# Kernel optimization log

Measured on AMD Instinct MI355X. Metric: run time of the kernel, lower is better.

The kernel has to match this reference:

```python
import jax, jax.numpy as jnp
import numpy as np

B, N, IN_DIM, OUT_DIM = 8, 2048, 128, 128
NEG_SLOPE = 0.2

def setup_inputs() -> dict:
    key = jax.random.key(0)
    k1, k2, k3, k4 = jax.random.split(key, 4)
    x = jax.random.normal(k1, (B, N, IN_DIM), dtype=jnp.float32)
    adj = jax.random.randint(k2, (N, N), 0, 2, dtype=jnp.int32)
    # nn.Linear weight init scale ~ 1/sqrt(fan_in)
    W = jax.random.normal(k3, (IN_DIM, OUT_DIM), dtype=jnp.float32) / np.sqrt(IN_DIM)
    a_vec = jax.random.normal(k4, (2 * OUT_DIM,), dtype=jnp.float32) / np.sqrt(2 * OUT_DIM)
    return {"x": x, "adj": adj, "W": W, "a_vec": a_vec}

def reference(x, adj, W, a_vec):
    # h = x @ W : [b, n, d]
    h = jnp.einsum("bni,io->bno", x, W)
    # Algebraic decomposition of a([h_i, h_j]) = a1.h_i + a2.h_j
    a1, a2 = a_vec[:OUT_DIM], a_vec[OUT_DIM:]
    s_i = h @ a1  # [b, n] score contribution from source node i
    s_j = h @ a2  # [b, n] score contribution from target node j
    e = s_i[:, :, None] + s_j[:, None, :]  # [b, n, n]
    e = jnp.where(e >= 0, e, NEG_SLOPE * e)  # leaky_relu(0.2)
    mask = (adj > 0)[None, :, :]  # [1, n, n] broadcast over batch
    e = jnp.where(mask, e, -jnp.inf)
    alpha = jax.nn.softmax(e, axis=-1)  # [b, n, n]
    out = jnp.einsum("bnm,bmd->bnd", alpha, h)  # [b, n, d]
    return out, alpha
```

## Files before the change

### kernel.cpp

```cpp
#include <hip/hip_runtime.h>
#include <hip/hip_bf16.h>
#include <cstdint>
#include <cstddef>

constexpr int Bn = 8;
constexpr int Nn = 2048;
constexpr int Dn = 128;

typedef __bf16 bf16x8 __attribute__((ext_vector_type(8)));
typedef float f32x4 __attribute__((ext_vector_type(4)));

#define AS1 __attribute__((address_space(1)))
#define AS3 __attribute__((address_space(3)))

static __device__ __forceinline__ void gl_lds16(const void* g, void* l) {
  __builtin_amdgcn_global_load_lds((AS1 const void*)g, (AS3 void*)l, 16, 0, 0);
}

__global__ __launch_bounds__(256) void gat_k0(
    const int* __restrict__ adj, unsigned long long* __restrict__ mask64) {
  const int t = threadIdx.x;
  const size_t g = (size_t)blockIdx.x * 256 + t;
  int v = adj[g];
  unsigned long long bal = __ballot(v > 0);
  if ((t & 63) == 0) mask64[g >> 6] = bal;
}

__global__ __launch_bounds__(256) void gat_k1(
    const float* __restrict__ x, const float* __restrict__ W,
    const float* __restrict__ a_vec,
    __bf16* __restrict__ hT, float* __restrict__ s1, float* __restrict__ s2) {
  __shared__ __align__(16) float Wl[64 * 144];
  __shared__ __align__(16) float xL[32 * 132];

  const int t = threadIdx.x;
  const int r0 = blockIdx.x * 32;
  const int b = r0 >> 11;
  const int n0 = r0 & (Nn - 1);
  const int rp = (t >> 4) << 1;
  const int c0 = (t & 15) << 3;
  const int c0p = c0 + ((c0 >> 5) << 2);

  float acc[2][8];
#pragma unroll
  for (int r = 0; r < 2; ++r)
#pragma unroll
    for (int c = 0; c < 8; ++c) acc[r][c] = 0.f;

#pragma unroll
  for (int it = 0; it < 4; ++it) {
    int idx = t + (it << 8);
    int rr = idx >> 5, kc = (idx & 31) << 2;
    *(float4*)(xL + rr * 132 + kc) = *(const float4*)(x + (size_t)(r0 + rr) * Dn + kc);
  }

  for (int ph = 0; ph < 2; ++ph) {
    if (ph) __syncthreads();
#pragma unroll
    for (int it = 0; it < 8; ++it) {
      int idx = t + (it << 8);
      int kk = idx >> 5, c4 = (idx & 31) << 2;
      int dsto = kk * 144 + c4 + ((c4 >> 5) << 2);
      *(float4*)(Wl + dsto) = *(const float4*)(W + (size_t)((ph << 6) + kk) * Dn + c4);
    }
    __syncthreads();
    const float* xrow = xL + rp * 132 + (ph << 6);
    for (int k = 0; k < 64; ++k) {
      float xa0 = xrow[k];
      float xa1 = xrow[132 + k];
      float4 w0 = *(const float4*)(Wl + k * 144 + c0p);
      float4 w1 = *(const float4*)(Wl + k * 144 + c0p + 4);
      float ws[8] = {w0.x, w0.y, w0.z, w0.w, w1.x, w1.y, w1.z, w1.w};
#pragma unroll
      for (int c = 0; c < 8; ++c) {
        acc[0][c] = fmaf(xa0, ws[c], acc[0][c]);
        acc[1][c] = fmaf(xa1, ws[c], acc[1][c]);
      }
    }
  }

  float q1[2] = {0.f, 0.f}, q2[2] = {0.f, 0.f};
#pragma unroll
  for (int c = 0; c < 8; ++c) {
    float a1c = a_vec[c0 + c];
    float a2c = a_vec[Dn + c0 + c];
    q1[0] = fmaf(acc[0][c], a1c, q1[0]);
    q1[1] = fmaf(acc[1][c], a1c, q1[1]);
    q2[0] = fmaf(acc[0][c], a2c, q2[0]);
    q2[1] = fmaf(acc[1][c], a2c, q2[1]);
  }
#pragma unroll
  for (int d = 1; d < 16; d <<= 1) {
    q1[0] += __shfl_xor(q1[0], d);
    q1[1] += __shfl_xor(q1[1], d);
    q2[0] += __shfl_xor(q2[0], d);
    q2[1] += __shfl_xor(q2[1], d);
  }
  if ((t & 15) == 0) {
    s1[b * Nn + n0 + rp] = q1[0];
    s1[b * Nn + n0 + rp + 1] = q1[1];
    s2[b * Nn + n0 + rp] = q2[0];
    s2[b * Nn + n0 + rp + 1] = q2[1];
  }

#pragma unroll
  for (int c = 0; c < 8; ++c) {
    union { __bf16 h[2]; uint32_t u; } pk;
    pk.h[0] = (__bf16)acc[0][c];
    pk.h[1] = (__bf16)acc[1][c];
    *(uint32_t*)(hT + (size_t)(b * Dn + c0 + c) * Nn + n0 + rp) = pk.u;
  }
}

__global__ __launch_bounds__(512) void gat_k2(
    const uint32_t* __restrict__ mask, const __bf16* __restrict__ hT,
    const float* __restrict__ s1, const float* __restrict__ s2,
    float* __restrict__ out, float* __restrict__ alpha) {
  __shared__ __align__(16) float sj[Nn];
  __shared__ float siv[32], invl[32];
  __shared__ __align__(16) __bf16 Pl[2][32 * 72];
  __shared__ __align__(16) __bf16 hl[2][128 * 64];

  const int t = threadIdx.x;
  const int b = blockIdx.x & 7;
  const int i0 = (blockIdx.x >> 3) << 5;
  const int w = t >> 6, lane = t & 63;
  const int ii = t >> 4, sub = t & 15;
  const int lrow = lane >> 3, ccs = lane & 7;
  const __bf16* __restrict__ hTb = hT + (size_t)b * Dn * Nn;

#pragma unroll
  for (int inst = 0; inst < 2; ++inst) {
    int row = (w << 4) + (inst << 3) + lrow;
    gl_lds16(hTb + (size_t)row * Nn + ((ccs ^ lrow) << 3),
             &hl[0][((w << 4) + (inst << 3)) << 6]);
  }

  *(float4*)(sj + (t << 2)) = *(const float4*)(s2 + b * Nn + (t << 2));
  if (t < 32) siv[t] = s1[b * Nn + i0 + t];
  __syncthreads();

  const int i = i0 + ii;
  const uint32_t* __restrict__ mrow = mask + ((size_t)i << 6);
  const float si = siv[ii];

  float l = 0.f;
  const int wofs = sub >> 3;
  const int bsh = (sub & 7) << 2;
  for (int cc = 0; cc < 32; ++cc) {
    int j = (cc << 6) + (sub << 2);
    uint32_t mw = mrow[(cc << 1) + wofs];
    float4 sv = *(const float4*)(sj + j);
    float e;
    e = si + sv.x; e = fmaxf(e, 0.2f * e); l += ((mw >> (bsh + 0)) & 1u) ? __expf(e) : 0.f;
    e = si + sv.y; e = fmaxf(e, 0.2f * e); l += ((mw >> (bsh + 1)) & 1u) ? __expf(e) : 0.f;
    e = si + sv.z; e = fmaxf(e, 0.2f * e); l += ((mw >> (bsh + 2)) & 1u) ? __expf(e) : 0.f;
    e = si + sv.w; e = fmaxf(e, 0.2f * e); l += ((mw >> (bsh + 3)) & 1u) ? __expf(e) : 0.f;
  }
  l += __shfl_xor(l, 1);
  l += __shfl_xor(l, 2);
  l += __shfl_xor(l, 4);
  l += __shfl_xor(l, 8);
  if (sub == 0) invl[ii] = 1.f / l;
  __syncthreads();
  const float il = invl[ii];

  const int iw = (w & 1) << 4;
  const int nd0 = (w >> 1) << 5;
  const int q16 = lane >> 4, m16 = lane & 15;
  f32x4 acc0 = {0.f, 0.f, 0.f, 0.f}, acc1 = {0.f, 0.f, 0.f, 0.f};
  float* __restrict__ arow = alpha + ((size_t)(b * Nn + i) << 11);

  for (int jt = 0; jt < 32; ++jt) {
    const int buf = jt & 1;
    const int j0 = jt << 6;
    {
      int j = j0 + (sub << 2);
      uint32_t mw = mrow[(j0 >> 5) + wofs];
      float4 sv = *(const float4*)(sj + j);
      float e0 = si + sv.x; e0 = fmaxf(e0, 0.2f * e0);
      float e1 = si + sv.y; e1 = fmaxf(e1, 0.2f * e1);
      float e2 = si + sv.z; e2 = fmaxf(e2, 0.2f * e2);
      float e3 = si + sv.w; e3 = fmaxf(e3, 0.2f * e3);
      float a0 = ((mw >> (bsh + 0)) & 1u) ? __expf(e0) * il : 0.f;
      float a1 = ((mw >> (bsh + 1)) & 1u) ? __expf(e1) * il : 0.f;
      float a2 = ((mw >> (bsh + 2)) & 1u) ? __expf(e2) * il : 0.f;
      float a3 = ((mw >> (bsh + 3)) & 1u) ? __expf(e3) * il : 0.f;
      *(float4*)(arow + j) = make_float4(a0, a1, a2, a3);
      union { __bf16 h[4]; uint2 u; } pk;
      pk.h[0] = (__bf16)a0; pk.h[1] = (__bf16)a1;
      pk.h[2] = (__bf16)a2; pk.h[3] = (__bf16)a3;
      *(uint2*)(&Pl[buf][ii * 72 + (sub << 2)]) = pk.u;
    }
    __syncthreads();
    if (jt < 31) {
      int jn = j0 + 64;
#pragma unroll
      for (int inst = 0; inst < 2; ++inst) {
        int row = (w << 4) + (inst << 3) + lrow;
        gl_lds16(hTb + (size_t)row * Nn + jn + ((ccs ^ lrow) << 3),
                 &hl[buf ^ 1][((w << 4) + (inst << 3)) << 6]);
      }
    }
#pragma unroll
    for (int ks = 0; ks < 2; ++ks) {
      bf16x8 af = *(const bf16x8*)(&Pl[buf][(iw + m16) * 72 + (ks << 5) + (q16 << 3)]);
      {
        int d = nd0 + m16;
        int phys = ((ks << 2) + q16) ^ (d & 7);
        bf16x8 bv = *(const bf16x8*)(&hl[buf][(d << 6) + (phys << 3)]);
        acc0 = __builtin_amdgcn_mfma_f32_16x16x32_bf16(af, bv, acc0, 0, 0, 0);
      }
      {
        int d = nd0 + 16 + m16;
        int phys = ((ks << 2) + q16) ^ (d & 7);
        bf16x8 bv = *(const bf16x8*)(&hl[buf][(d << 6) + (phys << 3)]);
        acc1 = __builtin_amdgcn_mfma_f32_16x16x32_bf16(af, bv, acc1, 0, 0, 0);
      }
    }
  }

#pragma unroll
  for (int nb = 0; nb < 2; ++nb) {
    f32x4 a = nb ? acc1 : acc0;
    int d = nd0 + (nb << 4) + m16;
#pragma unroll
    for (int r = 0; r < 4; ++r) {
      int irow = i0 + iw + (q16 << 2) + r;
      out[((size_t)(b * Nn + irow) << 7) + d] = a[r];
    }
  }
}

extern "C" void kernel_launch(void* const* d_in, const int* in_sizes, int n_in,
                              void* d_out, int out_size, void* d_ws, size_t ws_size,
                              hipStream_t stream) {
  const float* x = (const float*)d_in[0];
  const int* adj = (const int*)d_in[1];
  const float* W = (const float*)d_in[2];
  const float* a_vec = (const float*)d_in[3];

  float* out = (float*)d_out;
  float* alpha = out + (size_t)Bn * Nn * Dn;

  char* ws = (char*)d_ws;
  __bf16* hT = (__bf16*)ws;
  float* s1 = (float*)(ws + (size_t)Bn * Dn * Nn * 2);
  float* s2 = s1 + (size_t)Bn * Nn;
  unsigned long long* mask64 = (unsigned long long*)(s2 + (size_t)Bn * Nn);

  gat_k0<<<(Nn * Nn) / 256, 256, 0, stream>>>(adj, mask64);
  gat_k1<<<512, 256, 0, stream>>>(x, W, a_vec, hT, s1, s2);
  gat_k2<<<512, 512, 0, stream>>>((const uint32_t*)mask64, hT, s1, s2, out, alpha);
}
```

Before: 200.9 us.

## Split alpha writing into separate blocks and fuse mask packing into projection kernel

The adjacency mask packing moves into the projection kernel, so the standalone mask kernel disappears. The softmax row sums now come from a new small kernel that writes 1/l to the workspace. The main kernel no longer writes the 128 MB alpha matrix from its MFMA loop. Instead, 1024 extra blocks in the same launch recompute and write alpha with nontemporal stores, running in parallel with the P·h matmul blocks. The aim is to stop the large alpha store from stalling the matmul pipeline, at the cost of recomputing the exponentials and adding one more launch.

```diff
diff --git a/kernel.cpp b/kernel.cpp
--- a/kernel.cpp
+++ b/kernel.cpp
@@ -17,19 +17,11 @@
   __builtin_amdgcn_global_load_lds((AS1 const void*)g, (AS3 void*)l, 16, 0, 0);
 }
 
-__global__ __launch_bounds__(256) void gat_k0(
-    const int* __restrict__ adj, unsigned long long* __restrict__ mask64) {
-  const int t = threadIdx.x;
-  const size_t g = (size_t)blockIdx.x * 256 + t;
-  int v = adj[g];
-  unsigned long long bal = __ballot(v > 0);
-  if ((t & 63) == 0) mask64[g >> 6] = bal;
-}
-
 __global__ __launch_bounds__(256) void gat_k1(
     const float* __restrict__ x, const float* __restrict__ W,
-    const float* __restrict__ a_vec,
-    __bf16* __restrict__ hT, float* __restrict__ s1, float* __restrict__ s2) {
+    const float* __restrict__ a_vec, const int* __restrict__ adj,
+    __bf16* __restrict__ hT, float* __restrict__ s1, float* __restrict__ s2,
+    unsigned long long* __restrict__ mask64) {
   __shared__ __align__(16) float Wl[64 * 144];
   __shared__ __align__(16) float xL[32 * 132];
 
@@ -110,18 +102,96 @@
     pk.h[1] = (__bf16)acc[1][c];
     *(uint32_t*)(hT + (size_t)(b * Dn + c0 + c) * Nn + n0 + rp) = pk.u;
   }
-}
-
-__global__ __launch_bounds__(512) void gat_k2(
+
+  {
+    const size_t base = (size_t)blockIdx.x * 8192;
+#pragma unroll 4
+    for (int it = 0; it < 32; ++it) {
+      size_t g = base + (it << 8) + t;
+      int v = adj[g];
+      unsigned long long bal = __ballot(v > 0);
+      if ((t & 63) == 0) mask64[g >> 6] = bal;
+    }
+  }
+}
+
+__global__ __launch_bounds__(256) void gat_k2a(
+    const uint32_t* __restrict__ mask, const float* __restrict__ s1,
+    const float* __restrict__ s2, float* __restrict__ invl_g) {
+  __shared__ __align__(16) float sj[Nn];
+  const int t = threadIdx.x;
+  const int b = blockIdx.x & 7;
+  const int i0 = (blockIdx.x >> 3) << 5;
+#pragma unroll
+  for (int it = 0; it < 2; ++it) {
+    int idx = (t + (it << 8)) << 2;
+    *(float4*)(sj + idx) = *(const float4*)(s2 + b * Nn + idx);
+  }
+  __syncthreads();
+
+  const int ii = t >> 3, sub = t & 7;
+  const int i = i0 + ii;
+  const uint32_t* __restrict__ mrow = mask + ((size_t)i << 6);
+  const float si = s1[b * Nn + i];
+  const int bsh = sub << 2;
+
+  float l = 0.f;
+  for (int cc = 0; cc < 64; ++cc) {
+    uint32_t mw = mrow[cc];
+    float4 sv = *(const float4*)(sj + (cc << 5) + bsh);
+    float e;
+    e = si + sv.x; e = fmaxf(e, 0.2f * e); l += ((mw >> (bsh + 0)) & 1u) ? __expf(e) : 0.f;
+    e = si + sv.y; e = fmaxf(e, 0.2f * e); l += ((mw >> (bsh + 1)) & 1u) ? __expf(e) : 0.f;
+    e = si + sv.z; e = fmaxf(e, 0.2f * e); l += ((mw >> (bsh + 2)) & 1u) ? __expf(e) : 0.f;
+    e = si + sv.w; e = fmaxf(e, 0.2f * e); l += ((mw >> (bsh + 3)) & 1u) ? __expf(e) : 0.f;
+  }
+  l += __shfl_xor(l, 1);
+  l += __shfl_xor(l, 2);
+  l += __shfl_xor(l, 4);
+  if (sub == 0) invl_g[b * Nn + i] = 1.f / l;
+}
+
+__global__ __launch_bounds__(512) void gat_k2bc(
     const uint32_t* __restrict__ mask, const __bf16* __restrict__ hT,
     const float* __restrict__ s1, const float* __restrict__ s2,
+    const float* __restrict__ invl_g,
     float* __restrict__ out, float* __restrict__ alpha) {
   __shared__ __align__(16) float sj[Nn];
-  __shared__ float siv[32], invl[32];
+  __shared__ float siv[32], ilv[32];
   __shared__ __align__(16) __bf16 Pl[2][32 * 72];
   __shared__ __align__(16) __bf16 hl[2][128 * 64];
 
   const int t = threadIdx.x;
+
+  if (blockIdx.x >= 512) {
+    const int a = blockIdx.x - 512;
+    const int b = a & 7;
+    const int i0 = (a >> 3) << 4;
+    const int j0 = t << 2;
+    const float4 sv = *(const float4*)(s2 + b * Nn + j0);
+    const int wi = t >> 3, bsh = (t & 7) << 2;
+    float e0 = sv.x, e1 = sv.y, e2 = sv.z, e3 = sv.w;
+    float* __restrict__ arow = alpha + (((size_t)(b * Nn + i0)) << 11) + j0;
+#pragma unroll 2
+    for (int r = 0; r < 16; ++r) {
+      const int i = i0 + r;
+      const float si = s1[b * Nn + i];
+      const float il = invl_g[b * Nn + i];
+      const uint32_t mw = mask[((size_t)i << 6) + wi];
+      float a0 = si + e0; a0 = fmaxf(a0, 0.2f * a0);
+      float a1 = si + e1; a1 = fmaxf(a1, 0.2f * a1);
+      float a2 = si + e2; a2 = fmaxf(a2, 0.2f * a2);
+      float a3 = si + e3; a3 = fmaxf(a3, 0.2f * a3);
+      f32x4 av;
+      av.x = ((mw >> (bsh + 0)) & 1u) ? __expf(a0) * il : 0.f;
+      av.y = ((mw >> (bsh + 1)) & 1u) ? __expf(a1) * il : 0.f;
+      av.z = ((mw >> (bsh + 2)) & 1u) ? __expf(a2) * il : 0.f;
+      av.w = ((mw >> (bsh + 3)) & 1u) ? __expf(a3) * il : 0.f;
+      __builtin_nontemporal_store(av, (f32x4*)(arow + ((size_t)r << 11)));
+    }
+    return;
+  }
+
   const int b = blockIdx.x & 7;
   const int i0 = (blockIdx.x >> 3) << 5;
   const int w = t >> 6, lane = t & 63;
@@ -131,45 +201,28 @@
 
 #pragma unroll
   for (int inst = 0; inst < 2; ++inst) {
-    int row = (w << 4) + (inst << 3) + lrow;
-    gl_lds16(hTb + (size_t)row * Nn + ((ccs ^ lrow) << 3),
+    gl_lds16(hTb + (size_t)((w << 4) + (inst << 3) + lrow) * Nn + ((ccs ^ lrow) << 3),
              &hl[0][((w << 4) + (inst << 3)) << 6]);
   }
 
   *(float4*)(sj + (t << 2)) = *(const float4*)(s2 + b * Nn + (t << 2));
-  if (t < 32) siv[t] = s1[b * Nn + i0 + t];
+  if (t < 32) {
+    siv[t] = s1[b * Nn + i0 + t];
+    ilv[t] = invl_g[b * Nn + i0 + t];
+  }
   __syncthreads();
 
   const int i = i0 + ii;
   const uint32_t* __restrict__ mrow = mask + ((size_t)i << 6);
   const float si = siv[ii];
-
-  float l = 0.f;
+  const float il = ilv[ii];
   const int wofs = sub >> 3;
   const int bsh = (sub & 7) << 2;
-  for (int cc = 0; cc < 32; ++cc) {
-    int j = (cc << 6) + (sub << 2);
-    uint32_t mw = mrow[(cc << 1) + wofs];
-    float4 sv = *(const float4*)(sj + j);
-    float e;
-    e = si + sv.x; e = fmaxf(e, 0.2f * e); l += ((mw >> (bsh + 0)) & 1u) ? __expf(e) : 0.f;
-    e = si + sv.y; e = fmaxf(e, 0.2f * e); l += ((mw >> (bsh + 1)) & 1u) ? __expf(e) : 0.f;
-    e = si + sv.z; e = fmaxf(e, 0.2f * e); l += ((mw >> (bsh + 2)) & 1u) ? __expf(e) : 0.f;
-    e = si + sv.w; e = fmaxf(e, 0.2f * e); l += ((mw >> (bsh + 3)) & 1u) ? __expf(e) : 0.f;
-  }
-  l += __shfl_xor(l, 1);
-  l += __shfl_xor(l, 2);
-  l += __shfl_xor(l, 4);
-  l += __shfl_xor(l, 8);
-  if (sub == 0) invl[ii] = 1.f / l;
-  __syncthreads();
-  const float il = invl[ii];
 
   const int iw = (w & 1) << 4;
   const int nd0 = (w >> 1) << 5;
   const int q16 = lane >> 4, m16 = lane & 15;
   f32x4 acc0 = {0.f, 0.f, 0.f, 0.f}, acc1 = {0.f, 0.f, 0.f, 0.f};
-  float* __restrict__ arow = alpha + ((size_t)(b * Nn + i) << 11);
 
   for (int jt = 0; jt < 32; ++jt) {
     const int buf = jt & 1;
@@ -186,7 +239,6 @@
       float a1 = ((mw >> (bsh + 1)) & 1u) ? __expf(e1) * il : 0.f;
       float a2 = ((mw >> (bsh + 2)) & 1u) ? __expf(e2) * il : 0.f;
       float a3 = ((mw >> (bsh + 3)) & 1u) ? __expf(e3) * il : 0.f;
-      *(float4*)(arow + j) = make_float4(a0, a1, a2, a3);
       union { __bf16 h[4]; uint2 u; } pk;
       pk.h[0] = (__bf16)a0; pk.h[1] = (__bf16)a1;
       pk.h[2] = (__bf16)a2; pk.h[3] = (__bf16)a3;
@@ -197,8 +249,7 @@
       int jn = j0 + 64;
 #pragma unroll
       for (int inst = 0; inst < 2; ++inst) {
-        int row = (w << 4) + (inst << 3) + lrow;
-        gl_lds16(hTb + (size_t)row * Nn + jn + ((ccs ^ lrow) << 3),
+        gl_lds16(hTb + (size_t)((w << 4) + (inst << 3) + lrow) * Nn + jn + ((ccs ^ lrow) << 3),
                  &hl[buf ^ 1][((w << 4) + (inst << 3)) << 6]);
       }
     }
@@ -227,7 +278,7 @@
 #pragma unroll
     for (int r = 0; r < 4; ++r) {
       int irow = i0 + iw + (q16 << 2) + r;
-      out[((size_t)(b * Nn + irow) << 7) + d] = a[r];
+      __builtin_nontemporal_store(a[r], out + ((size_t)(b * Nn + irow) << 7) + d);
     }
   }
 }
@@ -247,9 +298,10 @@
   __bf16* hT = (__bf16*)ws;
   float* s1 = (float*)(ws + (size_t)Bn * Dn * Nn * 2);
   float* s2 = s1 + (size_t)Bn * Nn;
-  unsigned long long* mask64 = (unsigned long long*)(s2 + (size_t)Bn * Nn);
-
-  gat_k0<<<(Nn * Nn) / 256, 256, 0, stream>>>(adj, mask64);
-  gat_k1<<<512, 256, 0, stream>>>(x, W, a_vec, hT, s1, s2);
-  gat_k2<<<512, 512, 0, stream>>>((const uint32_t*)mask64, hT, s1, s2, out, alpha);
-}
+  float* invl = s2 + (size_t)Bn * Nn;
+  unsigned long long* mask64 = (unsigned long long*)(invl + (size_t)Bn * Nn);
+
+  gat_k1<<<512, 256, 0, stream>>>(x, W, a_vec, adj, hT, s1, s2, mask64);
+  gat_k2a<<<512, 256, 0, stream>>>((const uint32_t*)mask64, s1, s2, invl);
+  gat_k2bc<<<1536, 512, 0, stream>>>((const uint32_t*)mask64, hT, s1, s2, invl, out, alpha);
+}
```

Result: slower. 215.6 us (+7.3%).
